# Optimization experiments

Hardware: AMD Instinct MI355X
Metric: run time of the kernel (lower is better)

Reference implementation:

```python
import jax, jax.numpy as jnp
import numpy as np

H, N2, R = 512, 16, 32   # hidden_dim, state_dim//2, dt_rank=ceil(512/16)
B, L = 1, 4096


def setup_inputs() -> dict:
    key = jax.random.key(0)
    ks = jax.random.split(key, 7)
    u = jax.random.normal(ks[0], (B, L, H), dtype=jnp.float32)
    # Parameter initialization mirroring S4DKernel.__init__
    A_log = jnp.zeros((H, N2), jnp.float32)                      # log(ones)
    A_im = jnp.broadcast_to(jnp.arange(N2, dtype=jnp.float32), (H, N2)).copy()
    B_param = jax.random.normal(ks[1], (H, N2, 2), jnp.float32)
    C_param = jax.random.normal(ks[2], (H, N2, 2), jnp.float32)
    D = jax.random.normal(ks[3], (H,), jnp.float32)
    dt_w = jax.random.normal(ks[4], (H, R), jnp.float32) / np.sqrt(R)
    dt_min, dt_max, dt_floor = 1e-3, 0.1, 1e-4
    dt_init = jnp.exp(jax.random.uniform(ks[5], (H,), jnp.float32)
                      * (np.log(dt_max) - np.log(dt_floor)) + np.log(dt_floor))
    dt_init = jnp.maximum(dt_init, dt_min)
    dt_b = dt_init + jnp.log(-jnp.expm1(-dt_init))               # inverse-softplus init
    xproj_w = jax.random.normal(ks[6], (R, H), jnp.float32) / np.sqrt(H)
    return {"u": u, "A_log": A_log, "A_im": A_im, "B_param": B_param,
            "C_param": C_param, "D": D, "dt_w": dt_w, "dt_b": dt_b,
            "xproj_w": xproj_w}


def reference(u, A_log, A_im, B_param, C_param, D, dt_w, dt_b, xproj_w):
    # Complex continuous-time parameters
    A = -jnp.exp(A_log) + 1j * A_im                 # [H, N2]
    Bc = B_param[..., 0] + 1j * B_param[..., 1]     # [H, N2]
    Cc = C_param[..., 0] + 1j * C_param[..., 1]     # [H, N2]

    # dt path: x_proj_for_dt (no bias) -> dt_proj -> softplus
    dt_u = jnp.einsum('blh,rh->blr', u, xproj_w)                    # [B,L,R]
    dt = jax.nn.softplus(jnp.einsum('blr,hr->blh', dt_u, dt_w) + dt_b)  # [B,L,H]

    # ZOH discretization
    z = dt[..., None] * A                           # [B,L,H,N2] complex
    A_bar = jnp.exp(z)
    B_bar_div = jnp.where(jnp.abs(z) < 1e-4, 1.0 + z / 2, (jnp.exp(z) - 1.0) / z)
    ub = u[..., None].astype(A_bar.dtype) * B_bar_div * Bc          # [B,L,H,N2]

    # Parallel scan for h_k = A_k * h_{k-1} + u_k (first-order linear recurrence)
    def op(c1, c2):
        a1, b1 = c1
        a2, b2 = c2
        return a1 * a2, a2 * b1 + b2
    _, h = jax.lax.associative_scan(op, (A_bar, ub), axis=1)        # [B,L,H,N2]

    y = jnp.einsum('blhn,hn->blh', h, Cc) + u * D
    return y.real
```

## Files before the change

kernel.cpp:

```cpp
#include <hip/hip_runtime.h>

#define Hd 512
#define N2d 16
#define Rd 32
#define Ld 4096
#define NCHUNK 128
#define CLEN (Ld / NCHUNK)
#define NCH (Hd * N2d)

__global__ __launch_bounds__(256) void k_tw(const float* __restrict__ dt_w,
                                            float* __restrict__ dt_wT) {
    int idx = blockIdx.x * 256 + threadIdx.x;
    int r = idx >> 9;
    int h = idx & 511;
    dt_wT[idx] = dt_w[h * Rd + r];
}

__global__ __launch_bounds__(256) void k_dt(const float* __restrict__ u,
                                            const float* __restrict__ xproj_w,
                                            const float* __restrict__ dt_wT,
                                            const float* __restrict__ dt_b,
                                            float2* __restrict__ du_out) {
    __shared__ float u_s[8][Hd];
    __shared__ float dtu_s[8][Rd];
    const int t = threadIdx.x;
    const int l0 = blockIdx.x * 8;

    #pragma unroll
    for (int i = 0; i < 16; ++i) {
        int idx = t + i * 256;
        ((float*)u_s)[idx] = u[l0 * Hd + idx];
    }
    __syncthreads();

    const int r = t >> 3;
    const int j = t & 7;
    float part[8];
    #pragma unroll
    for (int l = 0; l < 8; ++l) part[l] = 0.f;
    for (int k = 0; k < 64; ++k) {
        float w = xproj_w[r * Hd + k * 8 + j];
        #pragma unroll
        for (int l = 0; l < 8; ++l) part[l] = fmaf(u_s[l][k * 8 + j], w, part[l]);
    }
    #pragma unroll
    for (int off = 1; off < 8; off <<= 1) {
        #pragma unroll
        for (int l = 0; l < 8; ++l) part[l] += __shfl_xor(part[l], off);
    }
    if (j == 0) {
        #pragma unroll
        for (int l = 0; l < 8; ++l) dtu_s[l][r] = part[l];
    }
    __syncthreads();

    #pragma unroll
    for (int hb = 0; hb < 2; ++hb) {
        int h = hb * 256 + t;
        float bias = dt_b[h];
        float acc[8];
        #pragma unroll
        for (int l = 0; l < 8; ++l) acc[l] = bias;
        for (int rr = 0; rr < Rd; ++rr) {
            float w = dt_wT[rr * Hd + h];
            #pragma unroll
            for (int l = 0; l < 8; ++l) acc[l] = fmaf(dtu_s[l][rr], w, acc[l]);
        }
        #pragma unroll
        for (int l = 0; l < 8; ++l) {
            float x = acc[l];
            float sp = fmaxf(x, 0.f) + log1pf(__expf(-fabsf(x)));
            float uv = u_s[l][h];
            float us = uv * __builtin_amdgcn_rcpf(fmaxf(sp, 1e-30f));
            du_out[(l0 + l) * Hd + h] = make_float2(sp, us);
        }
    }
}

__device__ __forceinline__ bool load_consts4(const float* A_log, const float* A_im,
        const float* B_param, int hnb,
        float* Are, float* Aim, float* BAr, float* BAi) {
    #pragma unroll
    for (int j = 0; j < 4; ++j) {
        int hn = hnb + j;
        Are[j] = -__expf(A_log[hn]);
        Aim[j] = A_im[hn];
        float Bre = B_param[2 * hn];
        float Bim = B_param[2 * hn + 1];
        float inv = __builtin_amdgcn_rcpf(Are[j] * Are[j] + Aim[j] * Aim[j]);
        BAr[j] = (Bre * Are[j] + Bim * Aim[j]) * inv;
        BAi[j] = (Bim * Are[j] - Bre * Aim[j]) * inv;
    }
    float d1 = Aim[1] - Aim[0], d2 = Aim[2] - Aim[1], d3 = Aim[3] - Aim[2];
    return (Are[1] == Are[0]) && (Are[2] == Are[0]) && (Are[3] == Are[0]) &&
           (d1 == d2) && (d2 == d3);
}

__global__ __launch_bounds__(256) void k_chunk(const float2* __restrict__ du,
        const float* __restrict__ A_log, const float* __restrict__ A_im,
        const float* __restrict__ B_param,
        float2* __restrict__ Pbuf, float2* __restrict__ Sbuf) {
    const int t = threadIdx.x;
    const int q = t & 3;
    const int h = blockIdx.y * 64 + (t >> 2);
    const int c = blockIdx.x;
    const int hnb = h * N2d + q * 4;
    float Are[4], Aim[4], BAr[4], BAi[4];
    const bool fast = load_consts4(A_log, A_im, B_param, hnb, Are, Aim, BAr, BAi);
    float sr[4] = {0.f, 0.f, 0.f, 0.f}, si[4] = {0.f, 0.f, 0.f, 0.f};
    float sdt = 0.f;
    const int lbase = c * CLEN;
    if (fast) {
        const float Are0 = Are[0], Aim0 = Aim[0], dA = Aim[1] - Aim[0];
        #pragma unroll 4
        for (int k = 0; k < CLEN; ++k) {
            float2 d = du[(lbase + k) * Hd + h];
            float dtv = d.x, us = d.y;
            sdt += dtv;
            float er = __expf(dtv * Are0);
            float s0, c0, sd, cd;
            __sincosf(dtv * Aim0, &s0, &c0);
            __sincosf(dtv * dA, &sd, &cd);
            float ar = er * c0, ai = er * s0;
            #pragma unroll
            for (int j = 0; j < 4; ++j) {
                float gr = fmaf(ar, us, -us);
                float gi = ai * us;
                float nr = fmaf(ar, sr[j], fmaf(-ai, si[j], fmaf(gr, BAr[j], -gi * BAi[j])));
                float ni = fmaf(ar, si[j], fmaf( ai, sr[j], fmaf(gr, BAi[j],  gi * BAr[j])));
                sr[j] = nr; si[j] = ni;
                if (j < 3) {
                    float tr = fmaf(ar, cd, -ai * sd);
                    ai = fmaf(ai, cd, ar * sd);
                    ar = tr;
                }
            }
        }
    } else {
        #pragma unroll 4
        for (int k = 0; k < CLEN; ++k) {
            float2 d = du[(lbase + k) * Hd + h];
            float dtv = d.x, us = d.y;
            sdt += dtv;
            #pragma unroll
            for (int j = 0; j < 4; ++j) {
                float er = __expf(dtv * Are[j]);
                float s, cc;
                __sincosf(dtv * Aim[j], &s, &cc);
                float ar = er * cc, ai = er * s;
                float gr = fmaf(ar, us, -us);
                float gi = ai * us;
                float nr = fmaf(ar, sr[j], fmaf(-ai, si[j], fmaf(gr, BAr[j], -gi * BAi[j])));
                float ni = fmaf(ar, si[j], fmaf( ai, sr[j], fmaf(gr, BAi[j],  gi * BAr[j])));
                sr[j] = nr; si[j] = ni;
            }
        }
    }
    int base = c * NCH + hnb;
    #pragma unroll
    for (int j = 0; j < 4; ++j) {
        float er = __expf(sdt * Are[j]);
        float s, cc;
        __sincosf(sdt * Aim[j], &s, &cc);
        Pbuf[base + j] = make_float2(er * cc, er * s);
        Sbuf[base + j] = make_float2(sr[j], si[j]);
    }
}

__global__ __launch_bounds__(256) void k_prefix(const float2* __restrict__ Pbuf,
        const float2* __restrict__ Sbuf, float2* __restrict__ Ibuf) {
    int idx = blockIdx.x * 256 + threadIdx.x;
    float hr = 0.f, hi = 0.f;
    for (int b = 0; b < NCHUNK / 8; ++b) {
        float2 tp[8], ts[8];
        #pragma unroll
        for (int i = 0; i < 8; ++i) {
            tp[i] = Pbuf[(b * 8 + i) * NCH + idx];
            ts[i] = Sbuf[(b * 8 + i) * NCH + idx];
        }
        #pragma unroll
        for (int i = 0; i < 8; ++i) {
            Ibuf[(b * 8 + i) * NCH + idx] = make_float2(hr, hi);
            float nr = fmaf(tp[i].x, hr, fmaf(-tp[i].y, hi, ts[i].x));
            float ni = fmaf(tp[i].x, hi, fmaf( tp[i].y, hr, ts[i].y));
            hr = nr; hi = ni;
        }
    }
}

__global__ __launch_bounds__(256) void k_scan(const float2* __restrict__ du,
        const float* __restrict__ A_log, const float* __restrict__ A_im,
        const float* __restrict__ B_param, const float* __restrict__ C_param,
        const float* __restrict__ Dp, const float2* __restrict__ Ibuf,
        float* __restrict__ out) {
    const int t = threadIdx.x;
    const int q = t & 3;
    const int h = blockIdx.y * 64 + (t >> 2);
    const int c = blockIdx.x;
    const int hnb = h * N2d + q * 4;
    float Are[4], Aim[4], BAr[4], BAi[4], Cre[4], Cim[4];
    const bool fast = load_consts4(A_log, A_im, B_param, hnb, Are, Aim, BAr, BAi);
    #pragma unroll
    for (int j = 0; j < 4; ++j) {
        Cre[j] = C_param[2 * (hnb + j)];
        Cim[j] = C_param[2 * (hnb + j) + 1];
    }
    const float Dv = Dp[h];
    float hr[4], hi[4];
    {
        int base = c * NCH + hnb;
        #pragma unroll
        for (int j = 0; j < 4; ++j) {
            float2 h0 = Ibuf[base + j];
            hr[j] = h0.x; hi[j] = h0.y;
        }
    }
    const int lbase = c * CLEN;
    if (fast) {
        const float Are0 = Are[0], Aim0 = Aim[0], dA = Aim[1] - Aim[0];
        #pragma unroll 4
        for (int k = 0; k < CLEN; ++k) {
            int l = lbase + k;
            float2 d = du[l * Hd + h];
            float dtv = d.x, us = d.y;
            float er = __expf(dtv * Are0);
            float s0, c0, sd, cd;
            __sincosf(dtv * Aim0, &s0, &c0);
            __sincosf(dtv * dA, &sd, &cd);
            float ar = er * c0, ai = er * s0;
            float yv = 0.f;
            #pragma unroll
            for (int j = 0; j < 4; ++j) {
                float gr = fmaf(ar, us, -us);
                float gi = ai * us;
                float nr = fmaf(ar, hr[j], fmaf(-ai, hi[j], fmaf(gr, BAr[j], -gi * BAi[j])));
                float ni = fmaf(ar, hi[j], fmaf( ai, hr[j], fmaf(gr, BAi[j],  gi * BAr[j])));
                hr[j] = nr; hi[j] = ni;
                yv = fmaf(nr, Cre[j], fmaf(-ni, Cim[j], yv));
                if (j < 3) {
                    float tr = fmaf(ar, cd, -ai * sd);
                    ai = fmaf(ai, cd, ar * sd);
                    ar = tr;
                }
            }
            yv += __shfl_xor(yv, 1);
            yv += __shfl_xor(yv, 2);
            if (q == 0) out[l * Hd + h] = fmaf(dtv * us, Dv, yv);
        }
    } else {
        #pragma unroll 4
        for (int k = 0; k < CLEN; ++k) {
            int l = lbase + k;
            float2 d = du[l * Hd + h];
            float dtv = d.x, us = d.y;
            float yv = 0.f;
            #pragma unroll
            for (int j = 0; j < 4; ++j) {
                float er = __expf(dtv * Are[j]);
                float s, cc;
                __sincosf(dtv * Aim[j], &s, &cc);
                float ar = er * cc, ai = er * s;
                float gr = fmaf(ar, us, -us);
                float gi = ai * us;
                float nr = fmaf(ar, hr[j], fmaf(-ai, hi[j], fmaf(gr, BAr[j], -gi * BAi[j])));
                float ni = fmaf(ar, hi[j], fmaf( ai, hr[j], fmaf(gr, BAi[j],  gi * BAr[j])));
                hr[j] = nr; hi[j] = ni;
                yv = fmaf(nr, Cre[j], fmaf(-ni, Cim[j], yv));
            }
            yv += __shfl_xor(yv, 1);
            yv += __shfl_xor(yv, 2);
            if (q == 0) out[l * Hd + h] = fmaf(dtv * us, Dv, yv);
        }
    }
}

extern "C" void kernel_launch(void* const* d_in, const int* in_sizes, int n_in,
                              void* d_out, int out_size, void* d_ws, size_t ws_size,
                              hipStream_t stream) {
    const float* u        = (const float*)d_in[0];
    const float* A_log    = (const float*)d_in[1];
    const float* A_im     = (const float*)d_in[2];
    const float* B_param  = (const float*)d_in[3];
    const float* C_param  = (const float*)d_in[4];
    const float* Dp       = (const float*)d_in[5];
    const float* dt_w     = (const float*)d_in[6];
    const float* dt_b     = (const float*)d_in[7];
    const float* xproj_w  = (const float*)d_in[8];

    float2* du   = (float2*)d_ws;
    float2* Pbuf = du + (size_t)Ld * Hd;
    float2* Sbuf = Pbuf + (size_t)NCHUNK * NCH;
    float2* Ibuf = Sbuf + (size_t)NCHUNK * NCH;
    float*  dt_wT = (float*)(Ibuf + (size_t)NCHUNK * NCH);
    float*  out  = (float*)d_out;

    k_tw<<<(Rd * Hd) / 256, 256, 0, stream>>>(dt_w, dt_wT);
    k_dt<<<Ld / 8, 256, 0, stream>>>(u, xproj_w, dt_wT, dt_b, du);
    dim3 g2(NCHUNK, Hd / 64);
    k_chunk<<<g2, 256, 0, stream>>>(du, A_log, A_im, B_param, Pbuf, Sbuf);
    k_prefix<<<NCH / 256, 256, 0, stream>>>(Pbuf, Sbuf, Ibuf);
    k_scan<<<g2, 256, 0, stream>>>(du, A_log, A_im, B_param, C_param, Dp, Ibuf, out);
}
```

Baseline: 152.7 us.

## Fuse dt, chunk, prefix and scan phases into one cooperative kernel

```diff
diff --git a/kernel.cpp b/kernel.cpp
--- a/kernel.cpp
+++ b/kernel.cpp
@@ -1,4 +1,7 @@
 #include <hip/hip_runtime.h>
+#include <hip/hip_cooperative_groups.h>
+
+namespace cg = cooperative_groups;
 
 #define Hd 512
 #define N2d 16
@@ -7,6 +10,8 @@
 #define NCHUNK 128
 #define CLEN (Ld / NCHUNK)
 #define NCH (Hd * N2d)
+#define PBLK 512
+#define VBLK 1024
 
 __global__ __launch_bounds__(256) void k_tw(const float* __restrict__ dt_w,
                                             float* __restrict__ dt_wT) {
@@ -14,67 +19,6 @@
     int r = idx >> 9;
     int h = idx & 511;
     dt_wT[idx] = dt_w[h * Rd + r];
-}
-
-__global__ __launch_bounds__(256) void k_dt(const float* __restrict__ u,
-                                            const float* __restrict__ xproj_w,
-                                            const float* __restrict__ dt_wT,
-                                            const float* __restrict__ dt_b,
-                                            float2* __restrict__ du_out) {
-    __shared__ float u_s[8][Hd];
-    __shared__ float dtu_s[8][Rd];
-    const int t = threadIdx.x;
-    const int l0 = blockIdx.x * 8;
-
-    #pragma unroll
-    for (int i = 0; i < 16; ++i) {
-        int idx = t + i * 256;
-        ((float*)u_s)[idx] = u[l0 * Hd + idx];
-    }
-    __syncthreads();
-
-    const int r = t >> 3;
-    const int j = t & 7;
-    float part[8];
-    #pragma unroll
-    for (int l = 0; l < 8; ++l) part[l] = 0.f;
-    for (int k = 0; k < 64; ++k) {
-        float w = xproj_w[r * Hd + k * 8 + j];
-        #pragma unroll
-        for (int l = 0; l < 8; ++l) part[l] = fmaf(u_s[l][k * 8 + j], w, part[l]);
-    }
-    #pragma unroll
-    for (int off = 1; off < 8; off <<= 1) {
-        #pragma unroll
-        for (int l = 0; l < 8; ++l) part[l] += __shfl_xor(part[l], off);
-    }
-    if (j == 0) {
-        #pragma unroll
-        for (int l = 0; l < 8; ++l) dtu_s[l][r] = part[l];
-    }
-    __syncthreads();
-
-    #pragma unroll
-    for (int hb = 0; hb < 2; ++hb) {
-        int h = hb * 256 + t;
-        float bias = dt_b[h];
-        float acc[8];
-        #pragma unroll
-        for (int l = 0; l < 8; ++l) acc[l] = bias;
-        for (int rr = 0; rr < Rd; ++rr) {
-            float w = dt_wT[rr * Hd + h];
-            #pragma unroll
-            for (int l = 0; l < 8; ++l) acc[l] = fmaf(dtu_s[l][rr], w, acc[l]);
-        }
-        #pragma unroll
-        for (int l = 0; l < 8; ++l) {
-            float x = acc[l];
-            float sp = fmaxf(x, 0.f) + log1pf(__expf(-fabsf(x)));
-            float uv = u_s[l][h];
-            float us = uv * __builtin_amdgcn_rcpf(fmaxf(sp, 1e-30f));
-            du_out[(l0 + l) * Hd + h] = make_float2(sp, us);
-        }
-    }
 }
 
 __device__ __forceinline__ bool load_consts4(const float* A_log, const float* A_im,
@@ -96,25 +40,78 @@
            (d1 == d2) && (d2 == d3);
 }
 
-__global__ __launch_bounds__(256) void k_chunk(const float2* __restrict__ du,
-        const float* __restrict__ A_log, const float* __restrict__ A_im,
-        const float* __restrict__ B_param,
-        float2* __restrict__ Pbuf, float2* __restrict__ Sbuf) {
-    const int t = threadIdx.x;
+__device__ __forceinline__ void phaseA(const float* __restrict__ u,
+        const float* __restrict__ xproj_w, const float* __restrict__ dt_wT,
+        const float* __restrict__ dt_b, float2* __restrict__ du,
+        int b, int t, float (*u_s)[Hd], float (*dtu_s)[Rd]) {
+    const int l0 = b * 8;
+    #pragma unroll
+    for (int i = 0; i < 16; ++i) {
+        int idx = t + i * 256;
+        ((float*)u_s)[idx] = u[l0 * Hd + idx];
+    }
+    __syncthreads();
+    const int r = t >> 3;
+    const int j = t & 7;
+    float part[8];
+    #pragma unroll
+    for (int l = 0; l < 8; ++l) part[l] = 0.f;
+    for (int k = 0; k < 64; ++k) {
+        float w = xproj_w[r * Hd + k * 8 + j];
+        #pragma unroll
+        for (int l = 0; l < 8; ++l) part[l] = fmaf(u_s[l][k * 8 + j], w, part[l]);
+    }
+    #pragma unroll
+    for (int off = 1; off < 8; off <<= 1) {
+        #pragma unroll
+        for (int l = 0; l < 8; ++l) part[l] += __shfl_xor(part[l], off);
+    }
+    if (j == 0) {
+        #pragma unroll
+        for (int l = 0; l < 8; ++l) dtu_s[l][r] = part[l];
+    }
+    __syncthreads();
+    #pragma unroll
+    for (int hb = 0; hb < 2; ++hb) {
+        int h = hb * 256 + t;
+        float bias = dt_b[h];
+        float acc[8];
+        #pragma unroll
+        for (int l = 0; l < 8; ++l) acc[l] = bias;
+        for (int rr = 0; rr < Rd; ++rr) {
+            float w = dt_wT[rr * Hd + h];
+            #pragma unroll
+            for (int l = 0; l < 8; ++l) acc[l] = fmaf(dtu_s[l][rr], w, acc[l]);
+        }
+        #pragma unroll
+        for (int l = 0; l < 8; ++l) {
+            float x = acc[l];
+            float sp = fmaxf(x, 0.f) + log1pf(__expf(-fabsf(x)));
+            float uv = u_s[l][h];
+            float us = uv * __builtin_amdgcn_rcpf(fmaxf(sp, 1e-30f));
+            du[(l0 + l) * Hd + h] = make_float2(sp, us);
+        }
+    }
+}
+
+__device__ __forceinline__ void phaseB(const float2* __restrict__ du,
+        const float* __restrict__ A_log, const float* __restrict__ A_im,
+        const float* __restrict__ B_param, float2* __restrict__ Pbuf,
+        float2* __restrict__ Sbuf, int vb, int t) {
     const int q = t & 3;
-    const int h = blockIdx.y * 64 + (t >> 2);
-    const int c = blockIdx.x;
-    const int hnb = h * N2d + q * 4;
+    const int hh = (vb >> 7) * 64 + (t >> 2);
+    const int c = vb & 127;
+    const int hnb = hh * N2d + q * 4;
+    const int lbase = c * CLEN;
     float Are[4], Aim[4], BAr[4], BAi[4];
     const bool fast = load_consts4(A_log, A_im, B_param, hnb, Are, Aim, BAr, BAi);
     float sr[4] = {0.f, 0.f, 0.f, 0.f}, si[4] = {0.f, 0.f, 0.f, 0.f};
     float sdt = 0.f;
-    const int lbase = c * CLEN;
     if (fast) {
         const float Are0 = Are[0], Aim0 = Aim[0], dA = Aim[1] - Aim[0];
         #pragma unroll 4
         for (int k = 0; k < CLEN; ++k) {
-            float2 d = du[(lbase + k) * Hd + h];
+            float2 d = du[(lbase + k) * Hd + hh];
             float dtv = d.x, us = d.y;
             sdt += dtv;
             float er = __expf(dtv * Are0);
@@ -123,13 +120,13 @@
             __sincosf(dtv * dA, &sd, &cd);
             float ar = er * c0, ai = er * s0;
             #pragma unroll
-            for (int j = 0; j < 4; ++j) {
+            for (int jj = 0; jj < 4; ++jj) {
                 float gr = fmaf(ar, us, -us);
                 float gi = ai * us;
-                float nr = fmaf(ar, sr[j], fmaf(-ai, si[j], fmaf(gr, BAr[j], -gi * BAi[j])));
-                float ni = fmaf(ar, si[j], fmaf( ai, sr[j], fmaf(gr, BAi[j],  gi * BAr[j])));
-                sr[j] = nr; si[j] = ni;
-                if (j < 3) {
+                float nr = fmaf(ar, sr[jj], fmaf(-ai, si[jj], fmaf(gr, BAr[jj], -gi * BAi[jj])));
+                float ni = fmaf(ar, si[jj], fmaf( ai, sr[jj], fmaf(gr, BAi[jj],  gi * BAr[jj])));
+                sr[jj] = nr; si[jj] = ni;
+                if (jj < 3) {
                     float tr = fmaf(ar, cd, -ai * sd);
                     ai = fmaf(ai, cd, ar * sd);
                     ar = tr;
@@ -139,48 +136,47 @@
     } else {
         #pragma unroll 4
         for (int k = 0; k < CLEN; ++k) {
-            float2 d = du[(lbase + k) * Hd + h];
+            float2 d = du[(lbase + k) * Hd + hh];
             float dtv = d.x, us = d.y;
             sdt += dtv;
             #pragma unroll
-            for (int j = 0; j < 4; ++j) {
-                float er = __expf(dtv * Are[j]);
+            for (int jj = 0; jj < 4; ++jj) {
+                float er = __expf(dtv * Are[jj]);
                 float s, cc;
-                __sincosf(dtv * Aim[j], &s, &cc);
+                __sincosf(dtv * Aim[jj], &s, &cc);
                 float ar = er * cc, ai = er * s;
                 float gr = fmaf(ar, us, -us);
                 float gi = ai * us;
-                float nr = fmaf(ar, sr[j], fmaf(-ai, si[j], fmaf(gr, BAr[j], -gi * BAi[j])));
-                float ni = fmaf(ar, si[j], fmaf( ai, sr[j], fmaf(gr, BAi[j],  gi * BAr[j])));
-                sr[j] = nr; si[j] = ni;
+                float nr = fmaf(ar, sr[jj], fmaf(-ai, si[jj], fmaf(gr, BAr[jj], -gi * BAi[jj])));
+                float ni = fmaf(ar, si[jj], fmaf( ai, sr[jj], fmaf(gr, BAi[jj],  gi * BAr[jj])));
+                sr[jj] = nr; si[jj] = ni;
             }
         }
     }
     int base = c * NCH + hnb;
     #pragma unroll
-    for (int j = 0; j < 4; ++j) {
-        float er = __expf(sdt * Are[j]);
+    for (int jj = 0; jj < 4; ++jj) {
+        float er = __expf(sdt * Are[jj]);
         float s, cc;
-        __sincosf(sdt * Aim[j], &s, &cc);
-        Pbuf[base + j] = make_float2(er * cc, er * s);
-        Sbuf[base + j] = make_float2(sr[j], si[j]);
-    }
-}
-
-__global__ __launch_bounds__(256) void k_prefix(const float2* __restrict__ Pbuf,
-        const float2* __restrict__ Sbuf, float2* __restrict__ Ibuf) {
-    int idx = blockIdx.x * 256 + threadIdx.x;
+        __sincosf(sdt * Aim[jj], &s, &cc);
+        Pbuf[base + jj] = make_float2(er * cc, er * s);
+        Sbuf[base + jj] = make_float2(sr[jj], si[jj]);
+    }
+}
+
+__device__ __forceinline__ void phaseC(const float2* __restrict__ Pbuf,
+        const float2* __restrict__ Sbuf, float2* __restrict__ Ibuf, int gidx) {
     float hr = 0.f, hi = 0.f;
-    for (int b = 0; b < NCHUNK / 8; ++b) {
+    for (int bb = 0; bb < NCHUNK / 8; ++bb) {
         float2 tp[8], ts[8];
         #pragma unroll
         for (int i = 0; i < 8; ++i) {
-            tp[i] = Pbuf[(b * 8 + i) * NCH + idx];
-            ts[i] = Sbuf[(b * 8 + i) * NCH + idx];
+            tp[i] = Pbuf[(bb * 8 + i) * NCH + gidx];
+            ts[i] = Sbuf[(bb * 8 + i) * NCH + gidx];
         }
         #pragma unroll
         for (int i = 0; i < 8; ++i) {
-            Ibuf[(b * 8 + i) * NCH + idx] = make_float2(hr, hi);
+            Ibuf[(bb * 8 + i) * NCH + gidx] = make_float2(hr, hi);
             float nr = fmaf(tp[i].x, hr, fmaf(-tp[i].y, hi, ts[i].x));
             float ni = fmaf(tp[i].x, hi, fmaf( tp[i].y, hr, ts[i].y));
             hr = nr; hi = ni;
@@ -188,40 +184,39 @@
     }
 }
 
-__global__ __launch_bounds__(256) void k_scan(const float2* __restrict__ du,
+__device__ __forceinline__ void phaseD(const float2* __restrict__ du,
         const float* __restrict__ A_log, const float* __restrict__ A_im,
         const float* __restrict__ B_param, const float* __restrict__ C_param,
         const float* __restrict__ Dp, const float2* __restrict__ Ibuf,
-        float* __restrict__ out) {
-    const int t = threadIdx.x;
+        float* __restrict__ out, int vb, int t) {
     const int q = t & 3;
-    const int h = blockIdx.y * 64 + (t >> 2);
-    const int c = blockIdx.x;
-    const int hnb = h * N2d + q * 4;
+    const int hh = (vb >> 7) * 64 + (t >> 2);
+    const int c = vb & 127;
+    const int hnb = hh * N2d + q * 4;
+    const int lbase = c * CLEN;
     float Are[4], Aim[4], BAr[4], BAi[4], Cre[4], Cim[4];
     const bool fast = load_consts4(A_log, A_im, B_param, hnb, Are, Aim, BAr, BAi);
     #pragma unroll
-    for (int j = 0; j < 4; ++j) {
-        Cre[j] = C_param[2 * (hnb + j)];
-        Cim[j] = C_param[2 * (hnb + j) + 1];
-    }
-    const float Dv = Dp[h];
+    for (int jj = 0; jj < 4; ++jj) {
+        Cre[jj] = C_param[2 * (hnb + jj)];
+        Cim[jj] = C_param[2 * (hnb + jj) + 1];
+    }
+    const float Dv = Dp[hh];
     float hr[4], hi[4];
     {
         int base = c * NCH + hnb;
         #pragma unroll
-        for (int j = 0; j < 4; ++j) {
-            float2 h0 = Ibuf[base + j];
-            hr[j] = h0.x; hi[j] = h0.y;
-        }
-    }
-    const int lbase = c * CLEN;
+        for (int jj = 0; jj < 4; ++jj) {
+            float2 h0 = Ibuf[base + jj];
+            hr[jj] = h0.x; hi[jj] = h0.y;
+        }
+    }
     if (fast) {
         const float Are0 = Are[0], Aim0 = Aim[0], dA = Aim[1] - Aim[0];
         #pragma unroll 4
         for (int k = 0; k < CLEN; ++k) {
             int l = lbase + k;
-            float2 d = du[l * Hd + h];
+            float2 d = du[l * Hd + hh];
             float dtv = d.x, us = d.y;
             float er = __expf(dtv * Are0);
             float s0, c0, sd, cd;
@@ -230,14 +225,14 @@
             float ar = er * c0, ai = er * s0;
             float yv = 0.f;
             #pragma unroll
-            for (int j = 0; j < 4; ++j) {
+            for (int jj = 0; jj < 4; ++jj) {
                 float gr = fmaf(ar, us, -us);
                 float gi = ai * us;
-                float nr = fmaf(ar, hr[j], fmaf(-ai, hi[j], fmaf(gr, BAr[j], -gi * BAi[j])));
-                float ni = fmaf(ar, hi[j], fmaf( ai, hr[j], fmaf(gr, BAi[j],  gi * BAr[j])));
-                hr[j] = nr; hi[j] = ni;
-                yv = fmaf(nr, Cre[j], fmaf(-ni, Cim[j], yv));
-                if (j < 3) {
+                float nr = fmaf(ar, hr[jj], fmaf(-ai, hi[jj], fmaf(gr, BAr[jj], -gi * BAi[jj])));
+                float ni = fmaf(ar, hi[jj], fmaf( ai, hr[jj], fmaf(gr, BAi[jj],  gi * BAr[jj])));
+                hr[jj] = nr; hi[jj] = ni;
+                yv = fmaf(nr, Cre[jj], fmaf(-ni, Cim[jj], yv));
+                if (jj < 3) {
                     float tr = fmaf(ar, cd, -ai * sd);
                     ai = fmaf(ai, cd, ar * sd);
                     ar = tr;
@@ -245,33 +240,89 @@
             }
             yv += __shfl_xor(yv, 1);
             yv += __shfl_xor(yv, 2);
-            if (q == 0) out[l * Hd + h] = fmaf(dtv * us, Dv, yv);
+            if (q == 0) out[l * Hd + hh] = fmaf(dtv * us, Dv, yv);
         }
     } else {
         #pragma unroll 4
         for (int k = 0; k < CLEN; ++k) {
             int l = lbase + k;
-            float2 d = du[l * Hd + h];
+            float2 d = du[l * Hd + hh];
             float dtv = d.x, us = d.y;
             float yv = 0.f;
             #pragma unroll
-            for (int j = 0; j < 4; ++j) {
-                float er = __expf(dtv * Are[j]);
+            for (int jj = 0; jj < 4; ++jj) {
+                float er = __expf(dtv * Are[jj]);
                 float s, cc;
-                __sincosf(dtv * Aim[j], &s, &cc);
+                __sincosf(dtv * Aim[jj], &s, &cc);
                 float ar = er * cc, ai = er * s;
                 float gr = fmaf(ar, us, -us);
                 float gi = ai * us;
-                float nr = fmaf(ar, hr[j], fmaf(-ai, hi[j], fmaf(gr, BAr[j], -gi * BAi[j])));
-                float ni = fmaf(ar, hi[j], fmaf( ai, hr[j], fmaf(gr, BAi[j],  gi * BAr[j])));
-                hr[j] = nr; hi[j] = ni;
-                yv = fmaf(nr, Cre[j], fmaf(-ni, Cim[j], yv));
+                float nr = fmaf(ar, hr[jj], fmaf(-ai, hi[jj], fmaf(gr, BAr[jj], -gi * BAi[jj])));
+                float ni = fmaf(ar, hi[jj], fmaf( ai, hr[jj], fmaf(gr, BAi[jj],  gi * BAr[jj])));
+                hr[jj] = nr; hi[jj] = ni;
+                yv = fmaf(nr, Cre[jj], fmaf(-ni, Cim[jj], yv));
             }
             yv += __shfl_xor(yv, 1);
             yv += __shfl_xor(yv, 2);
-            if (q == 0) out[l * Hd + h] = fmaf(dtv * us, Dv, yv);
-        }
-    }
+            if (q == 0) out[l * Hd + hh] = fmaf(dtv * us, Dv, yv);
+        }
+    }
+}
+
+__global__ __launch_bounds__(256, 2) void k_fused(
+        const float* __restrict__ u, const float* __restrict__ xproj_w,
+        const float* __restrict__ dt_wT, const float* __restrict__ dt_b,
+        const float* __restrict__ A_log, const float* __restrict__ A_im,
+        const float* __restrict__ B_param, const float* __restrict__ C_param,
+        const float* __restrict__ Dp,
+        float2* __restrict__ du, float2* __restrict__ Pbuf,
+        float2* __restrict__ Sbuf, float2* __restrict__ Ibuf,
+        float* __restrict__ out) {
+    cg::grid_group grid = cg::this_grid();
+    __shared__ float u_s[8][Hd];
+    __shared__ float dtu_s[8][Rd];
+    const int t = threadIdx.x;
+    const int b = blockIdx.x;
+
+    phaseA(u, xproj_w, dt_wT, dt_b, du, b, t, u_s, dtu_s);
+    grid.sync();
+    phaseB(du, A_log, A_im, B_param, Pbuf, Sbuf, b, t);
+    phaseB(du, A_log, A_im, B_param, Pbuf, Sbuf, b + PBLK, t);
+    grid.sync();
+    if (b < NCH / 256) phaseC(Pbuf, Sbuf, Ibuf, b * 256 + t);
+    grid.sync();
+    phaseD(du, A_log, A_im, B_param, C_param, Dp, Ibuf, out, b, t);
+    phaseD(du, A_log, A_im, B_param, C_param, Dp, Ibuf, out, b + PBLK, t);
+}
+
+__global__ __launch_bounds__(256) void k_dt(const float* __restrict__ u,
+        const float* __restrict__ xproj_w, const float* __restrict__ dt_wT,
+        const float* __restrict__ dt_b, float2* __restrict__ du) {
+    __shared__ float u_s[8][Hd];
+    __shared__ float dtu_s[8][Rd];
+    phaseA(u, xproj_w, dt_wT, dt_b, du, blockIdx.x, threadIdx.x, u_s, dtu_s);
+}
+
+__global__ __launch_bounds__(256) void k_chunk(const float2* __restrict__ du,
+        const float* __restrict__ A_log, const float* __restrict__ A_im,
+        const float* __restrict__ B_param,
+        float2* __restrict__ Pbuf, float2* __restrict__ Sbuf) {
+    phaseB(du, A_log, A_im, B_param, Pbuf, Sbuf,
+           blockIdx.y * NCHUNK + blockIdx.x, threadIdx.x);
+}
+
+__global__ __launch_bounds__(256) void k_prefix(const float2* __restrict__ Pbuf,
+        const float2* __restrict__ Sbuf, float2* __restrict__ Ibuf) {
+    phaseC(Pbuf, Sbuf, Ibuf, blockIdx.x * 256 + threadIdx.x);
+}
+
+__global__ __launch_bounds__(256) void k_scan(const float2* __restrict__ du,
+        const float* __restrict__ A_log, const float* __restrict__ A_im,
+        const float* __restrict__ B_param, const float* __restrict__ C_param,
+        const float* __restrict__ Dp, const float2* __restrict__ Ibuf,
+        float* __restrict__ out) {
+    phaseD(du, A_log, A_im, B_param, C_param, Dp, Ibuf, out,
+           blockIdx.y * NCHUNK + blockIdx.x, threadIdx.x);
 }
 
 extern "C" void kernel_launch(void* const* d_in, const int* in_sizes, int n_in,
@@ -287,17 +338,27 @@
     const float* dt_b     = (const float*)d_in[7];
     const float* xproj_w  = (const float*)d_in[8];
 
-    float2* du   = (float2*)d_ws;
-    float2* Pbuf = du + (size_t)Ld * Hd;
-    float2* Sbuf = Pbuf + (size_t)NCHUNK * NCH;
-    float2* Ibuf = Sbuf + (size_t)NCHUNK * NCH;
+    float2* du    = (float2*)d_ws;
+    float2* Pbuf  = du + (size_t)Ld * Hd;
+    float2* Sbuf  = Pbuf + (size_t)NCHUNK * NCH;
+    float2* Ibuf  = Sbuf + (size_t)NCHUNK * NCH;
     float*  dt_wT = (float*)(Ibuf + (size_t)NCHUNK * NCH);
-    float*  out  = (float*)d_out;
+    float*  out   = (float*)d_out;
 
     k_tw<<<(Rd * Hd) / 256, 256, 0, stream>>>(dt_w, dt_wT);
-    k_dt<<<Ld / 8, 256, 0, stream>>>(u, xproj_w, dt_wT, dt_b, du);
-    dim3 g2(NCHUNK, Hd / 64);
-    k_chunk<<<g2, 256, 0, stream>>>(du, A_log, A_im, B_param, Pbuf, Sbuf);
-    k_prefix<<<NCH / 256, 256, 0, stream>>>(Pbuf, Sbuf, Ibuf);
-    k_scan<<<g2, 256, 0, stream>>>(du, A_log, A_im, B_param, C_param, Dp, Ibuf, out);
-}
+
+    void* args[] = { (void*)&u, (void*)&xproj_w, (void*)&dt_wT, (void*)&dt_b,
+                     (void*)&A_log, (void*)&A_im, (void*)&B_param, (void*)&C_param,
+                     (void*)&Dp, (void*)&du, (void*)&Pbuf, (void*)&Sbuf,
+                     (void*)&Ibuf, (void*)&out };
+    hipError_t ce = hipLaunchCooperativeKernel((void*)k_fused, dim3(PBLK),
+                                               dim3(256), args, 0, stream);
+    if (ce != hipSuccess) {
+        (void)hipGetLastError();
+        k_dt<<<Ld / 8, 256, 0, stream>>>(u, xproj_w, dt_wT, dt_b, du);
+        dim3 g2(NCHUNK, Hd / 64);
+        k_chunk<<<g2, 256, 0, stream>>>(du, A_log, A_im, B_param, Pbuf, Sbuf);
+        k_prefix<<<NCH / 256, 256, 0, stream>>>(Pbuf, Sbuf, Ibuf);
+        k_scan<<<g2, 256, 0, stream>>>(du, A_log, A_im, B_param, C_param, Dp, Ibuf, out);
+    }
+}
```

After: 341.8 us. 2.24x slower.
